# Performance work log

Measured on AMD Instinct MI355X. Metric: run time of the kernel, lower is better.

Reference implementation:

```python
import jax, jax.numpy as jnp
import numpy as np

N_POINTS = 262144   # rays x samples
N_VERTS = 6890      # SMPL vertex count
N_JOINTS = 24       # SMPL joints
CHUNK = 8192        # KNN query chunk size (keeps dist matrix at CHUNK x N_VERTS)


def _make_transforms(key, n):
    # Near-identity affine 4x4s (blend of these stays well-conditioned, like real
    # SMPL bone transforms which are rotations + translations).
    k1, k2 = jax.random.split(key)
    R = jnp.eye(3, dtype=jnp.float32) + 0.1 * jax.random.normal(k1, (n, 3, 3), jnp.float32)
    t = 0.1 * jax.random.normal(k2, (n, 3, 1), jnp.float32)
    top = jnp.concatenate([R, t], axis=2)                                   # [n,3,4]
    bot = jnp.tile(jnp.array([[[0.0, 0.0, 0.0, 1.0]]], jnp.float32), (n, 1, 1))
    return jnp.concatenate([top, bot], axis=1)                              # [n,4,4]


def setup_inputs() -> dict:
    key = jax.random.key(0)
    ks = jax.random.split(key, 5)
    query_pts = jax.random.normal(ks[0], (N_POINTS, 3), jnp.float32)
    verts = jax.random.normal(ks[1], (N_VERTS, 3), jnp.float32)
    w = jax.random.uniform(ks[2], (N_VERTS, N_JOINTS), jnp.float32)
    weights = w / jnp.sum(w, axis=1, keepdims=True)   # convex blend weights like SMPL
    A_t = _make_transforms(ks[3], N_JOINTS)
    A_big = _make_transforms(ks[4], N_JOINTS)
    return {"query_pts": query_pts, "verts": verts, "weights": weights,
            "A_t": A_t, "A_big": A_big}


def _nn_indices(query_pts, verts):
    # knn_points(..., K=1): nearest SMPL vertex per query point, chunked over queries.
    v_sq = jnp.sum(verts * verts, axis=1)  # [V]
    vT = verts.T                            # [3,V]

    def chunk_nn(q):  # q: [CHUNK,3]
        d = jnp.sum(q * q, axis=1, keepdims=True) - 2.0 * (q @ vT) + v_sq[None, :]
        return jnp.argmin(d, axis=1)

    qc = query_pts.reshape(-1, CHUNK, 3)
    idx = jax.lax.map(chunk_nn, qc).reshape(-1)  # [N]
    return jax.lax.stop_gradient(idx)            # vert_ids.detach() in torch


def reference(query_pts, verts, weights, A_t, A_big):
    idx = _nn_indices(query_pts, verts)
    bw = weights[idx]                                 # [N,24] gather of blend weights
    # A = bweights @ t_A.reshape(24,16) -> [N,4,4]
    A = jnp.einsum('nk,kij->nij', bw, A_t)
    can = query_pts - A[:, :3, 3]                     # remove translation
    R_inv = jnp.linalg.inv(A[:, :3, :3])              # per-point 3x3 inverse
    can = jnp.einsum('nij,nj->ni', R_inv, can)        # sum(R_inv * can[:,None], dim=2)
    # big-pose transform back out of canonical
    A2 = jnp.einsum('nk,kij->nij', bw, A_big)
    can = jnp.einsum('nij,nj->ni', A2[:, :3, :3], can) + A2[:, :3, 3]
    return can
```

## Files before the change

### kernel.cpp

```cpp
#include <hip/hip_runtime.h>

#define NPTS    262144
#define NV      6890
#define NCHUNK  4
#define CHUNKV  1728
#define NVP     (NCHUNK * CHUNKV)
#define NJ      24
#define PPL     4
#define WGS     256
#define NPG     (NPTS / (WGS * PPL))
#define NWG     (NPG * NCHUNK)

__global__ void pack_verts_kernel(const float* __restrict__ verts, float4* __restrict__ vp) {
    int v = blockIdx.x * 256 + threadIdx.x;
    if (v >= NVP) return;
    if (v < NV) {
        float x = verts[3*v+0], y = verts[3*v+1], z = verts[3*v+2];
        float vs = __fadd_rn(__fadd_rn(__fmul_rn(x,x), __fmul_rn(y,y)), __fmul_rn(z,z));
        vp[v] = make_float4(-2.f*x, -2.f*y, -2.f*z, vs);
    } else {
        vp[v] = make_float4(0.f, 0.f, 0.f, 3.0e37f);
    }
}

__global__ __launch_bounds__(WGS, 4)
void knn_kernel(const float* __restrict__ qpts,
                const float4* __restrict__ vp,
                float* __restrict__ bestp,
                int*   __restrict__ idxp)
{
    __shared__ float4 sv[CHUNKV];
    const int tid   = threadIdx.x;
    const int wg    = blockIdx.x;
    const int chunk = wg & (NCHUNK - 1);
    const int pg    = wg >> 2;
    const int vbase = chunk * CHUNKV;
    const int n0    = pg * (WGS * PPL) + tid;

    for (int i = tid; i < CHUNKV; i += WGS)
        sv[i] = vp[vbase + i];

    float q0[PPL], q1[PPL], q2[PPL];
#pragma unroll
    for (int p = 0; p < PPL; ++p) {
        const int n = n0 + p * WGS;
        q0[p] = qpts[3*n+0]; q1[p] = qpts[3*n+1]; q2[p] = qpts[3*n+2];
    }
    float best[PPL]; int bi[PPL];
#pragma unroll
    for (int p = 0; p < PPL; ++p) { best[p] = 3.4e38f; bi[p] = vbase; }

    __syncthreads();

#pragma unroll 8
    for (int u = 0; u < CHUNKV; ++u) {
        const float4 vv = sv[u];
        const int cand = vbase + u;
#pragma unroll
        for (int p = 0; p < PPL; ++p) {
            const float d = fmaf(vv.x, q0[p], fmaf(vv.y, q1[p], fmaf(vv.z, q2[p], vv.w)));
            const bool lt = d < best[p];
            best[p] = lt ? d : best[p];
            bi[p]   = lt ? cand : bi[p];
        }
    }

#pragma unroll
    for (int p = 0; p < PPL; ++p) {
        const int n = n0 + p * WGS;
        bestp[(size_t)chunk * NPTS + n] = best[p];
        idxp [(size_t)chunk * NPTS + n] = bi[p];
    }
}

template<int HAVE_IDX>
__global__ __launch_bounds__(256)
void blend_kernel(const float* __restrict__ qpts,
                  const float* __restrict__ verts,
                  const float* __restrict__ weights,
                  const float* __restrict__ At,
                  const float* __restrict__ Ab,
                  const float* __restrict__ bestp,
                  const int*   __restrict__ idxp,
                  float* __restrict__ out)
{
    __shared__ float sAt[NJ*16];
    __shared__ float sAb[NJ*16];
    const int tid = threadIdx.x;
    for (int i = tid; i < NJ*16; i += 256) { sAt[i] = At[i]; sAb[i] = Ab[i]; }

    const int n = blockIdx.x * 256 + tid;
    const float q0 = qpts[3*n+0], q1 = qpts[3*n+1], q2 = qpts[3*n+2];

    int bi;
    if (HAVE_IDX) {
        float bb = bestp[n];
        bi = idxp[n];
#pragma unroll
        for (int c = 1; c < NCHUNK; ++c) {
            const float bc = bestp[(size_t)c * NPTS + n];
            const int   ic = idxp [(size_t)c * NPTS + n];
            const bool lt = bc < bb;
            bb = lt ? bc : bb;
            bi = lt ? ic : bi;
        }
        __syncthreads();
    } else {
        const float qsq = __fadd_rn(__fadd_rn(__fmul_rn(q0,q0), __fmul_rn(q1,q1)), __fmul_rn(q2,q2));
        float best = 3.4e38f; bi = 0;
        for (int v = 0; v < NV; ++v) {
            float vx = verts[3*v+0], vy = verts[3*v+1], vz = verts[3*v+2];
            float vs = __fadd_rn(__fadd_rn(__fmul_rn(vx,vx), __fmul_rn(vy,vy)), __fmul_rn(vz,vz));
            float tq = fmaf(q2, vz, fmaf(q1, vy, __fmul_rn(q0, vx)));
            float d  = __fadd_rn(__fsub_rn(qsq, __fadd_rn(tq, tq)), vs);
            bool lt = d < best;
            best = lt ? d : best;
            bi   = lt ? v : bi;
        }
        __syncthreads();
    }

    const float4* wrow4 = (const float4*)(weights + (size_t)bi * NJ);
    float wv[NJ];
#pragma unroll
    for (int j = 0; j < 6; ++j) {
        float4 w4 = wrow4[j];
        wv[4*j+0] = w4.x; wv[4*j+1] = w4.y; wv[4*j+2] = w4.z; wv[4*j+3] = w4.w;
    }

    float M1[12], M2[12];
#pragma unroll
    for (int i = 0; i < 12; ++i) { M1[i] = 0.f; M2[i] = 0.f; }
#pragma unroll
    for (int k = 0; k < NJ; ++k) {
        const float w = wv[k];
        const float* a = sAt + k*16;
        const float* b = sAb + k*16;
#pragma unroll
        for (int i = 0; i < 12; ++i) {
            M1[i] = fmaf(w, a[i], M1[i]);
            M2[i] = fmaf(w, b[i], M2[i]);
        }
    }

    float p0 = q0 - M1[3], p1 = q1 - M1[7], p2 = q2 - M1[11];
    float a_=M1[0], b_=M1[1], c_=M1[2];
    float d_=M1[4], e_=M1[5], f_=M1[6];
    float g_=M1[8], h_=M1[9], i_=M1[10];
    float A0 = e_*i_ - f_*h_, A1 = c_*h_ - b_*i_, A2 = b_*f_ - c_*e_;
    float A3 = f_*g_ - d_*i_, A4 = a_*i_ - c_*g_, A5 = c_*d_ - a_*f_;
    float A6 = d_*h_ - e_*g_, A7 = b_*g_ - a_*h_, A8 = a_*e_ - b_*d_;
    float det  = a_*A0 + b_*A3 + c_*A6;
    float rdet = 1.0f / det;
    float x0 = (A0*p0 + A1*p1 + A2*p2) * rdet;
    float x1 = (A3*p0 + A4*p1 + A5*p2) * rdet;
    float x2 = (A6*p0 + A7*p1 + A8*p2) * rdet;

    out[3*n+0] = fmaf(M2[0],x0, fmaf(M2[1],x1, fmaf(M2[2], x2, M2[3])));
    out[3*n+1] = fmaf(M2[4],x0, fmaf(M2[5],x1, fmaf(M2[6], x2, M2[7])));
    out[3*n+2] = fmaf(M2[8],x0, fmaf(M2[9],x1, fmaf(M2[10],x2, M2[11])));
}

extern "C" void kernel_launch(void* const* d_in, const int* in_sizes, int n_in,
                              void* d_out, int out_size, void* d_ws, size_t ws_size,
                              hipStream_t stream) {
    const float* qpts    = (const float*)d_in[0];
    const float* verts   = (const float*)d_in[1];
    const float* weights = (const float*)d_in[2];
    const float* At      = (const float*)d_in[3];
    const float* Ab      = (const float*)d_in[4];
    float* out = (float*)d_out;

    const size_t vp_bytes   = (size_t)NVP * sizeof(float4);
    const size_t best_bytes = (size_t)NCHUNK * NPTS * sizeof(float);
    const size_t idx_bytes  = (size_t)NCHUNK * NPTS * sizeof(int);
    const size_t need = vp_bytes + best_bytes + idx_bytes;
    if (ws_size >= need) {
        float4* vp   = (float4*)d_ws;
        float* bestp = (float*)((char*)d_ws + vp_bytes);
        int*   idxp  = (int*)((char*)d_ws + vp_bytes + best_bytes);
        pack_verts_kernel<<<(NVP + 255) / 256, 256, 0, stream>>>(verts, vp);
        knn_kernel<<<NWG, WGS, 0, stream>>>(qpts, vp, bestp, idxp);
        blend_kernel<1><<<NPTS / 256, 256, 0, stream>>>(qpts, verts, weights, At, Ab, bestp, idxp, out);
    } else {
        blend_kernel<0><<<NPTS / 256, 256, 0, stream>>>(qpts, verts, weights, At, Ab, nullptr, nullptr, out);
    }
}
```

Measured before the change: 315.9 us.

## Split KNN into 8 vertex chunks, 8 points per lane, store 16-bit local indices

Doubles the number of vertex chunks and the points handled per thread, so each shared-memory vertex load is reused across eight queries. The per-chunk argmin is written with inline asm (one compare plus two cndmask), and only a 16-bit local index is stored per chunk. The blend kernel recomputes each chunk winner's distance from the packed vertices to merge chunks, which removes the float distance buffer. This cuts LDS traffic and scratch memory traffic, at the cost of more registers per thread and a small gather in the blend pass.

```diff
diff --git a/kernel.cpp b/kernel.cpp
--- a/kernel.cpp
+++ b/kernel.cpp
@@ -2,11 +2,11 @@
 
 #define NPTS    262144
 #define NV      6890
-#define NCHUNK  4
-#define CHUNKV  1728
+#define NCHUNK  8
+#define CHUNKV  864
 #define NVP     (NCHUNK * CHUNKV)
 #define NJ      24
-#define PPL     4
+#define PPL     8
 #define WGS     256
 #define NPG     (NPTS / (WGS * PPL))
 #define NWG     (NPG * NCHUNK)
@@ -26,14 +26,13 @@
 __global__ __launch_bounds__(WGS, 4)
 void knn_kernel(const float* __restrict__ qpts,
                 const float4* __restrict__ vp,
-                float* __restrict__ bestp,
-                int*   __restrict__ idxp)
+                unsigned short* __restrict__ idxp)
 {
     __shared__ float4 sv[CHUNKV];
     const int tid   = threadIdx.x;
     const int wg    = blockIdx.x;
     const int chunk = wg & (NCHUNK - 1);
-    const int pg    = wg >> 2;
+    const int pg    = wg >> 3;
     const int vbase = chunk * CHUNKV;
     const int n0    = pg * (WGS * PPL) + tid;
 
@@ -48,29 +47,29 @@
     }
     float best[PPL]; int bi[PPL];
 #pragma unroll
-    for (int p = 0; p < PPL; ++p) { best[p] = 3.4e38f; bi[p] = vbase; }
+    for (int p = 0; p < PPL; ++p) { best[p] = 3.4e38f; bi[p] = 0; }
 
     __syncthreads();
 
 #pragma unroll 8
     for (int u = 0; u < CHUNKV; ++u) {
         const float4 vv = sv[u];
-        const int cand = vbase + u;
+        int cand = u;
 #pragma unroll
         for (int p = 0; p < PPL; ++p) {
             const float d = fmaf(vv.x, q0[p], fmaf(vv.y, q1[p], fmaf(vv.z, q2[p], vv.w)));
-            const bool lt = d < best[p];
-            best[p] = lt ? d : best[p];
-            bi[p]   = lt ? cand : bi[p];
+            asm("v_cmp_lt_f32 vcc, %2, %0\n\t"
+                "v_cndmask_b32 %0, %0, %2, vcc\n\t"
+                "v_cndmask_b32 %1, %1, %3, vcc"
+                : "+v"(best[p]), "+v"(bi[p])
+                : "v"(d), "v"(cand)
+                : "vcc");
         }
     }
 
 #pragma unroll
-    for (int p = 0; p < PPL; ++p) {
-        const int n = n0 + p * WGS;
-        bestp[(size_t)chunk * NPTS + n] = best[p];
-        idxp [(size_t)chunk * NPTS + n] = bi[p];
-    }
+    for (int p = 0; p < PPL; ++p)
+        idxp[(size_t)chunk * NPTS + n0 + p * WGS] = (unsigned short)bi[p];
 }
 
 template<int HAVE_IDX>
@@ -80,8 +79,8 @@
                   const float* __restrict__ weights,
                   const float* __restrict__ At,
                   const float* __restrict__ Ab,
-                  const float* __restrict__ bestp,
-                  const int*   __restrict__ idxp,
+                  const unsigned short* __restrict__ idxp,
+                  const float4* __restrict__ vp,
                   float* __restrict__ out)
 {
     __shared__ float sAt[NJ*16];
@@ -94,28 +93,29 @@
 
     int bi;
     if (HAVE_IDX) {
-        float bb = bestp[n];
-        bi = idxp[n];
+        float bb = 3.4e38f; bi = 0;
 #pragma unroll
-        for (int c = 1; c < NCHUNK; ++c) {
-            const float bc = bestp[(size_t)c * NPTS + n];
-            const int   ic = idxp [(size_t)c * NPTS + n];
-            const bool lt = bc < bb;
-            bb = lt ? bc : bb;
-            bi = lt ? ic : bi;
+        for (int c = 0; c < NCHUNK; ++c) {
+            const int loc = idxp[(size_t)c * NPTS + n];
+            const int gi  = c * CHUNKV + loc;
+            const float4 vv = vp[gi];
+            const float d = fmaf(vv.x, q0, fmaf(vv.y, q1, fmaf(vv.z, q2, vv.w)));
+            const bool lt = d < bb;
+            bb = lt ? d : bb;
+            bi = lt ? gi : bi;
         }
         __syncthreads();
     } else {
         const float qsq = __fadd_rn(__fadd_rn(__fmul_rn(q0,q0), __fmul_rn(q1,q1)), __fmul_rn(q2,q2));
-        float best = 3.4e38f; bi = 0;
+        float bbest = 3.4e38f; bi = 0;
         for (int v = 0; v < NV; ++v) {
             float vx = verts[3*v+0], vy = verts[3*v+1], vz = verts[3*v+2];
             float vs = __fadd_rn(__fadd_rn(__fmul_rn(vx,vx), __fmul_rn(vy,vy)), __fmul_rn(vz,vz));
             float tq = fmaf(q2, vz, fmaf(q1, vy, __fmul_rn(q0, vx)));
             float d  = __fadd_rn(__fsub_rn(qsq, __fadd_rn(tq, tq)), vs);
-            bool lt = d < best;
-            best = lt ? d : best;
-            bi   = lt ? v : bi;
+            bool lt = d < bbest;
+            bbest = lt ? d : bbest;
+            bi    = lt ? v : bi;
         }
         __syncthreads();
     }
@@ -171,17 +171,15 @@
     const float* Ab      = (const float*)d_in[4];
     float* out = (float*)d_out;
 
-    const size_t vp_bytes   = (size_t)NVP * sizeof(float4);
-    const size_t best_bytes = (size_t)NCHUNK * NPTS * sizeof(float);
-    const size_t idx_bytes  = (size_t)NCHUNK * NPTS * sizeof(int);
-    const size_t need = vp_bytes + best_bytes + idx_bytes;
+    const size_t vp_bytes  = (size_t)NVP * sizeof(float4);
+    const size_t idx_bytes = (size_t)NCHUNK * NPTS * sizeof(unsigned short);
+    const size_t need = vp_bytes + idx_bytes;
     if (ws_size >= need) {
-        float4* vp   = (float4*)d_ws;
-        float* bestp = (float*)((char*)d_ws + vp_bytes);
-        int*   idxp  = (int*)((char*)d_ws + vp_bytes + best_bytes);
+        float4* vp = (float4*)d_ws;
+        unsigned short* idxp = (unsigned short*)((char*)d_ws + vp_bytes);
         pack_verts_kernel<<<(NVP + 255) / 256, 256, 0, stream>>>(verts, vp);
-        knn_kernel<<<NWG, WGS, 0, stream>>>(qpts, vp, bestp, idxp);
-        blend_kernel<1><<<NPTS / 256, 256, 0, stream>>>(qpts, verts, weights, At, Ab, bestp, idxp, out);
+        knn_kernel<<<NWG, WGS, 0, stream>>>(qpts, vp, idxp);
+        blend_kernel<1><<<NPTS / 256, 256, 0, stream>>>(qpts, verts, weights, At, Ab, idxp, vp, out);
     } else {
         blend_kernel<0><<<NPTS / 256, 256, 0, stream>>>(qpts, verts, weights, At, Ab, nullptr, nullptr, out);
     }
```

Measured after the change: 277.6 us. 1.14x faster.
